# Performance work log

Measured on AMD Instinct MI355X. Metric: run time of the kernel, lower is better.

Reference implementation:

```python
import jax, jax.numpy as jnp
import numpy as np

NEG = -1e9
THRESH = 0.97


def _gat(x, emask, W, al, ar, b):
    # x: [B,N,Fin], emask: [B,N,N] bool (src,dst), W: [Fin,H*D], al/ar: [H,D], b: [H*D]
    B, N, _ = x.shape
    H, D = al.shape
    feat = (x @ W).reshape(B, N, H, D)
    el = jnp.einsum('bnhd,hd->bnh', feat, al)
    er = jnp.einsum('bnhd,hd->bnh', feat, ar)
    # DGL GATConv: e = leaky_relu(el[src] + er[dst]); edge softmax over incoming edges of dst
    e = jax.nn.leaky_relu(el[:, :, None, :] + er[:, None, :, :], 0.2)  # [B,src,dst,H]
    e = jnp.where(emask[..., None], e, NEG)
    a = jnp.where(emask[..., None], jax.nn.softmax(e, axis=1), 0.0)  # softmax over src
    rst = jnp.einsum('bsdh,bshf->bdhf', a, feat).reshape(B, N, H * D)
    return jax.nn.elu(rst + b)


def _sem_attention(z, nmask, W1, b1, W2):
    # z: [B,N,M,Dz]; masked mean over all valid nodes of the batched graph (== DGL batch semantics)
    p = jnp.tanh(z @ W1 + b1) @ W2  # [B,N,M,1]
    w = (p * nmask[:, :, None, None]).sum(axis=(0, 1)) / nmask.sum()  # [M,1]
    beta = jax.nn.softmax(w, axis=0)  # [M,1]
    return (beta[None, None] * z).sum(axis=2)  # [B,N,Dz]


def _han_layer(h, emasks, nmask, fc, al, ar, b, sW1, sb1, sW2):
    M = fc.shape[0]
    embs = [_gat(h, emasks[m], fc[m], al[m], ar[m], b[m]) for m in range(M)]
    z = jnp.stack(embs, axis=2)  # [B,N,M,H*D]
    return _sem_attention(z, nmask, sW1, sb1, sW2)


def setup_inputs() -> dict:
    key = jax.random.key(0)
    ks = jax.random.split(key, 24)
    B, M, N, Fin = 4, 5, 1000, 64
    H, D = 4, 64
    HD = H * D  # 256
    SH = 128    # semantic attention hidden
    OUT = 5
    s = 0.1
    inp = {
        'x': jax.random.normal(ks[0], (B, M, N, Fin), dtype=jnp.float32),
        'adj': jax.random.uniform(ks[1], (B, M, N, N), dtype=jnp.float32),
        'node_nums': jax.random.randint(ks[2], (B,), 0, N),
        # layer 1 (in = Fin)
        'gat_fc1': jax.random.normal(ks[3], (M, Fin, HD), dtype=jnp.float32) * s,
        'gat_al1': jax.random.normal(ks[4], (M, H, D), dtype=jnp.float32) * s,
        'gat_ar1': jax.random.normal(ks[5], (M, H, D), dtype=jnp.float32) * s,
        'gat_b1': jnp.zeros((M, HD), dtype=jnp.float32),
        'sem_W1_1': jax.random.normal(ks[6], (HD, SH), dtype=jnp.float32) * s,
        'sem_b1_1': jnp.zeros((SH,), dtype=jnp.float32),
        'sem_W2_1': jax.random.normal(ks[7], (SH, 1), dtype=jnp.float32) * s,
        # layer 2 (in = HD)
        'gat_fc2': jax.random.normal(ks[8], (M, HD, HD), dtype=jnp.float32) * s,
        'gat_al2': jax.random.normal(ks[9], (M, H, D), dtype=jnp.float32) * s,
        'gat_ar2': jax.random.normal(ks[10], (M, H, D), dtype=jnp.float32) * s,
        'gat_b2': jnp.zeros((M, HD), dtype=jnp.float32),
        'sem_W1_2': jax.random.normal(ks[11], (HD, SH), dtype=jnp.float32) * s,
        'sem_b1_2': jnp.zeros((SH,), dtype=jnp.float32),
        'sem_W2_2': jax.random.normal(ks[12], (SH, 1), dtype=jnp.float32) * s,
        # prediction head
        'pred_W': jax.random.normal(ks[13], (HD, OUT), dtype=jnp.float32) * s,
        'pred_b': jnp.zeros((OUT,), dtype=jnp.float32),
    }
    return inp


def reference(x, adj, node_nums, gat_fc1, gat_al1, gat_ar1, gat_b1,
              sem_W1_1, sem_b1_1, sem_W2_1,
              gat_fc2, gat_al2, gat_ar2, gat_b2,
              sem_W1_2, sem_b1_2, sem_W2_2,
              pred_W, pred_b):
    B, M, N, Fin = x.shape
    h = x[:, 0]  # original cat-then-[0]: only channel-0 features are used
    nmask = (jnp.arange(N)[None, :] < node_nums[:, None]).astype(x.dtype)  # [B,N]
    pair = (nmask[:, :, None] * nmask[:, None, :]) > 0  # [B,N,N]
    emasks = [(adj[:, m] > THRESH) & pair for m in range(M)]
    h = _han_layer(h, emasks, nmask, gat_fc1, gat_al1, gat_ar1, gat_b1,
                   sem_W1_1, sem_b1_1, sem_W2_1)
    h = _han_layer(h, emasks, nmask, gat_fc2, gat_al2, gat_ar2, gat_b2,
                   sem_W1_2, sem_b1_2, sem_W2_2)
    logits = (h @ pred_W + pred_b) * nmask[:, :, None]  # scatter into padded [B,N,OUT]
    return logits
```

## Files before the change

### kernel.cpp

```cpp
#include <hip/hip_runtime.h>
#include <hip/hip_bf16.h>

#define B_ 4
#define M_ 5
#define N_ 1000
#define FIN 64
#define H_ 4
#define D_ 64
#define HD 256
#define SH 128
#define OUTD 5
#define NW 16
#define THRESH_ 0.97f

typedef unsigned short u16;
typedef u16 us8 __attribute__((ext_vector_type(8)));
typedef short s16x8 __attribute__((ext_vector_type(8)));
typedef float f32x4 __attribute__((ext_vector_type(4)));

__device__ inline u16 bf16_bits(float v) {
  __hip_bfloat16 h = __float2bfloat16(v);
  return *reinterpret_cast<u16*>(&h);
}
__device__ inline float bf16_val(u16 b) {
  __hip_bfloat16 h;
  *reinterpret_cast<u16*>(&h) = b;
  return __bfloat162float(h);
}
__device__ inline float b2f(u16 u) {
  union { unsigned int i; float f; } c;
  c.i = ((unsigned int)u) << 16;
  return c.f;
}
__device__ inline void split2(float v, u16& h, u16& l) {
  h = bf16_bits(v);
  l = bf16_bits(v - bf16_val(h));
}
__device__ inline void beta_from_sums(const float* __restrict__ psum,
                                      const int* __restrict__ node_nums,
                                      float* bb) {
  float tot = (float)(node_nums[0] + node_nums[1] + node_nums[2] + node_nums[3]);
  float w[M_], mx = -1e30f;
#pragma unroll
  for (int m = 0; m < M_; ++m) {
    w[m] = psum[m] / tot;
    mx = fmaxf(mx, w[m]);
  }
  float s = 0.f;
#pragma unroll
  for (int m = 0; m < M_; ++m) {
    w[m] = __expf(w[m] - mx);
    s += w[m];
  }
  float inv = 1.f / s;
#pragma unroll
  for (int m = 0; m < M_; ++m) bb[m] = w[m] * inv;
}

__device__ void splitT_body(const float* __restrict__ s, u16* __restrict__ hiT,
                            u16* __restrict__ loT, int K, int N, int k0, int n0,
                            char* smem) {
  float(*tile)[33] = (float(*)[33])smem;
  int tid = threadIdx.x;
  int kl = tid >> 3, nq = (tid & 7) * 4;
  *(float4*)&tile[kl][nq] = *(const float4*)(s + (size_t)(k0 + kl) * N + n0 + nq);
  __syncthreads();
  int nl = tid >> 3, kq = (tid & 7) * 4;
  ushort4 h, l;
  split2(tile[kq + 0][nl], h.x, l.x);
  split2(tile[kq + 1][nl], h.y, l.y);
  split2(tile[kq + 2][nl], h.z, l.z);
  split2(tile[kq + 3][nl], h.w, l.w);
  size_t o = (size_t)(n0 + nl) * K + k0 + kq;
  *(ushort4*)(hiT + o) = h;
  *(ushort4*)(loT + o) = l;
}

__global__ __launch_bounds__(256) void prep_all(
    const float* __restrict__ adj, const int* __restrict__ node_nums,
    unsigned long long* __restrict__ maskW,
    const float* __restrict__ fc1, u16* __restrict__ fc1Th, u16* __restrict__ fc1Tl,
    const float* __restrict__ fc2, u16* __restrict__ fc2Th, u16* __restrict__ fc2Tl,
    const float* __restrict__ sW1_1, u16* __restrict__ sW1Th1, u16* __restrict__ sW1Tl1,
    const float* __restrict__ sW1_2, u16* __restrict__ sW1Th2, u16* __restrict__ sW1Tl2) {
  __shared__ __align__(16) char smem[4608];
  int bi = blockIdx.x;
  int tid = threadIdx.x;
  if (bi < 5120) {
    int bx = bi & 15, by = (bi >> 4) & 15, bm = bi >> 8;
    int b = bm / M_;
    int s0 = bx * 64, d0 = by * 64;
    int nn = node_nums[b];
    unsigned char(*tile)[65] = (unsigned char(*)[65])smem;
    const float* arow = adj + (size_t)bm * N_ * N_;
#pragma unroll
    for (int k = 0; k < 16; ++k) {
      int idx = k * 256 + tid;
      int sl = idx >> 6, dl = idx & 63;
      int s = s0 + sl, d = d0 + dl;
      unsigned char v = 0;
      if (s < nn && d < nn && s < N_ && d < N_)
        v = (arow[(size_t)s * N_ + d] > THRESH_) ? 1 : 0;
      tile[sl][dl] = v;
    }
    __syncthreads();
    int w = tid >> 6, lane = tid & 63;
#pragma unroll
    for (int j = 0; j < 16; ++j) {
      int dl = w * 16 + j;
      bool act = tile[lane][dl] != 0;
      unsigned long long word = __ballot(act);
      int d = d0 + dl;
      if (lane == 0 && d < N_)
        maskW[((size_t)bm * N_ + d) * NW + bx] = word;
    }
    return;
  }
  bi -= 5120;
  if (bi < 80) {
    int kx = bi % 2, ny = (bi / 2) % 8, z = bi / 16;
    splitT_body(fc1 + (size_t)z * FIN * HD, fc1Th + (size_t)z * HD * FIN,
                fc1Tl + (size_t)z * HD * FIN, FIN, HD, kx * 32, ny * 32, smem);
    return;
  }
  bi -= 80;
  if (bi < 320) {
    int kx = bi % 8, ny = (bi / 8) % 8, z = bi / 64;
    splitT_body(fc2 + (size_t)z * HD * HD, fc2Th + (size_t)z * HD * HD,
                fc2Tl + (size_t)z * HD * HD, HD, HD, kx * 32, ny * 32, smem);
    return;
  }
  bi -= 320;
  if (bi < 32) {
    int kx = bi % 8, ny = bi / 8;
    splitT_body(sW1_1, sW1Th1, sW1Tl1, HD, SH, kx * 32, ny * 32, smem);
    return;
  }
  bi -= 32;
  {
    int kx = bi % 8, ny = bi / 8;
    splitT_body(sW1_2, sW1Th2, sW1Tl2, HD, SH, kx * 32, ny * 32, smem);
  }
}

__global__ __launch_bounds__(256) void gemm_mfma3(
    const float* __restrict__ A, int Mz, size_t aZ,
    const u16* __restrict__ Bh, const u16* __restrict__ Bl, size_t bZ,
    float* __restrict__ C, u16* __restrict__ Cbf, size_t cZ,
    int Mrows, int K, int Nc,
    const float* __restrict__ al, const float* __restrict__ ar,
    float* __restrict__ el, float* __restrict__ er) {
  __shared__ u16 sAh[64][40], sAl[64][40], sBh[64][40], sBl[64][40];
  __shared__ float elbuf[64][2], erbuf[64][2];
  int z = blockIdx.z;
  int b = z / Mz, m = z % Mz;
  const float* Ab = A + (size_t)b * aZ;
  const u16* Bhb = Bh + (size_t)m * bZ;
  const u16* Blb = Bl + (size_t)m * bZ;
  float* Cb = C + (size_t)z * cZ;
  u16* Cfb = Cbf + (size_t)z * cZ;
  int row0 = blockIdx.x * 64, col0 = blockIdx.y * 64;
  int tid = threadIdx.x;
  int arow = tid >> 2, akq = (tid & 3) * 8;
  int wid = tid >> 6, lane = tid & 63;
  int wr = (wid >> 1) * 32, wc = (wid & 1) * 32;
  int lrow = lane & 15, kseg = (lane >> 4) * 8;
  f32x4 zero4 = {0.f, 0.f, 0.f, 0.f};
  f32x4 acc[2][2];
  acc[0][0] = zero4; acc[0][1] = zero4; acc[1][0] = zero4; acc[1][1] = zero4;
  for (int k0 = 0; k0 < K; k0 += 32) {
    float4 a0 = make_float4(0.f, 0.f, 0.f, 0.f), a1 = a0;
    int gr = row0 + arow;
    if (gr < Mrows) {
      const float* ap = Ab + (size_t)gr * K + k0 + akq;
      a0 = *(const float4*)ap;
      a1 = *(const float4*)(ap + 4);
    }
    us8 hv, lv;
    {
      u16 th, tl;
      split2(a0.x, th, tl); hv[0] = th; lv[0] = tl;
      split2(a0.y, th, tl); hv[1] = th; lv[1] = tl;
      split2(a0.z, th, tl); hv[2] = th; lv[2] = tl;
      split2(a0.w, th, tl); hv[3] = th; lv[3] = tl;
      split2(a1.x, th, tl); hv[4] = th; lv[4] = tl;
      split2(a1.y, th, tl); hv[5] = th; lv[5] = tl;
      split2(a1.z, th, tl); hv[6] = th; lv[6] = tl;
      split2(a1.w, th, tl); hv[7] = th; lv[7] = tl;
    }
    *(us8*)&sAh[arow][akq] = hv;
    *(us8*)&sAl[arow][akq] = lv;
    us8 bv = *(const us8*)(Bhb + (size_t)(col0 + arow) * K + k0 + akq);
    us8 blv = *(const us8*)(Blb + (size_t)(col0 + arow) * K + k0 + akq);
    *(us8*)&sBh[arow][akq] = bv;
    *(us8*)&sBl[arow][akq] = blv;
    __syncthreads();
    s16x8 aH[2], aL[2], bH[2], bL[2];
#pragma unroll
    for (int i = 0; i < 2; ++i) {
      aH[i] = *(const s16x8*)&sAh[wr + 16 * i + lrow][kseg];
      aL[i] = *(const s16x8*)&sAl[wr + 16 * i + lrow][kseg];
      bH[i] = *(const s16x8*)&sBh[wc + 16 * i + lrow][kseg];
      bL[i] = *(const s16x8*)&sBl[wc + 16 * i + lrow][kseg];
    }
#pragma unroll
    for (int i = 0; i < 2; ++i)
#pragma unroll
      for (int j = 0; j < 2; ++j) {
        acc[i][j] = __builtin_amdgcn_mfma_f32_16x16x32_bf16(aH[i], bH[j], acc[i][j], 0, 0, 0);
        acc[i][j] = __builtin_amdgcn_mfma_f32_16x16x32_bf16(aH[i], bL[j], acc[i][j], 0, 0, 0);
        acc[i][j] = __builtin_amdgcn_mfma_f32_16x16x32_bf16(aL[i], bH[j], acc[i][j], 0, 0, 0);
      }
    __syncthreads();
  }
#pragma unroll
  for (int i = 0; i < 2; ++i)
#pragma unroll
    for (int j = 0; j < 2; ++j) {
      int ccol = col0 + wc + 16 * j + lrow;
#pragma unroll
      for (int r = 0; r < 4; ++r) {
        int crow = row0 + wr + 16 * i + (lane >> 4) * 4 + r;
        if (crow < Mrows) {
          float v = acc[i][j][r];
          Cb[(size_t)crow * Nc + ccol] = v;
          Cfb[(size_t)crow * Nc + ccol] = bf16_bits(v);
        }
      }
    }
  float alv0 = al[m * HD + col0 + wc + lrow];
  float alv1 = al[m * HD + col0 + wc + 16 + lrow];
  float arv0 = ar[m * HD + col0 + wc + lrow];
  float arv1 = ar[m * HD + col0 + wc + 16 + lrow];
#pragma unroll
  for (int i = 0; i < 2; ++i)
#pragma unroll
    for (int r = 0; r < 4; ++r) {
      float pl = acc[i][0][r] * alv0 + acc[i][1][r] * alv1;
      float pr = acc[i][0][r] * arv0 + acc[i][1][r] * arv1;
#pragma unroll
      for (int s = 1; s < 16; s <<= 1) {
        pl += __shfl_xor(pl, s, 64);
        pr += __shfl_xor(pr, s, 64);
      }
      if (lrow == 0) {
        int rl = wr + 16 * i + (lane >> 4) * 4 + r;
        elbuf[rl][wc >> 5] = pl;
        erbuf[rl][wc >> 5] = pr;
      }
    }
  __syncthreads();
  if (tid < 64) {
    int grow = row0 + tid;
    if (grow < Mrows) {
      int h = col0 >> 6;
      size_t bmN = (size_t)(b * M_ + m) * N_;
      el[(bmN + grow) * H_ + h] = elbuf[tid][0] + elbuf[tid][1];
      er[(bmN + grow) * H_ + h] = erbuf[tid][0] + erbuf[tid][1];
    }
  }
}

__global__ __launch_bounds__(256) void gat_agg(
    const unsigned long long* __restrict__ maskW, const u16* __restrict__ featbf,
    const float* __restrict__ el, const float* __restrict__ er,
    const float* __restrict__ gb, float* __restrict__ zout,
    u16* __restrict__ zbh, float* __restrict__ psum) {
  int wid = threadIdx.x >> 6, lane = threadIdx.x & 63;
  const int NWGQ = (B_ * M_ * N_ / 4) / 8;
  int orig = blockIdx.x;
  if (orig == 0 && threadIdx.x < 8) psum[threadIdx.x] = 0.f;
  int bid = (orig & 7) * NWGQ + (orig >> 3);
  int gw = bid * 4 + wid;
  int d = gw % N_, bm = gw / N_;
  int m = bm % M_, b = bm / M_;
  __shared__ int slist_all[4][1024];
  int* slist = slist_all[wid];

  const unsigned long long* mrow = maskW + ((size_t)bm * N_ + d) * NW;
  int cnt = 0;
#pragma unroll
  for (int q = 0; q < NW / 2; ++q) {
    ulonglong2 wp = *(const ulonglong2*)(mrow + q * 2);
    unsigned long long w0 = wp.x, w1 = wp.y;
    if (w0) {
      if ((w0 >> lane) & 1ull) {
        int pos = cnt + (int)__popcll(w0 & ((1ull << lane) - 1ull));
        slist[pos] = q * 128 + lane;
      }
      cnt += (int)__popcll(w0);
    }
    if (w1) {
      if ((w1 >> lane) & 1ull) {
        int pos = cnt + (int)__popcll(w1 & ((1ull << lane) - 1ull));
        slist[pos] = q * 128 + 64 + lane;
      }
      cnt += (int)__popcll(w1);
    }
  }

  int h = lane >> 4;
  float4 bias4 = *(const float4*)(gb + m * HD + lane * 4);
  size_t zoff = ((size_t)(b * N_ + d) * M_ + m) * HD + lane * 4;
  float4 o;
  if (cnt == 0) {
    o.x = bias4.x > 0.f ? bias4.x : (__expf(bias4.x) - 1.f);
    o.y = bias4.y > 0.f ? bias4.y : (__expf(bias4.y) - 1.f);
    o.z = bias4.z > 0.f ? bias4.z : (__expf(bias4.z) - 1.f);
    o.w = bias4.w > 0.f ? bias4.w : (__expf(bias4.w) - 1.f);
  } else {
    if (lane < 4) slist[cnt + lane] = slist[0];
    size_t bmN = (size_t)bm * N_;
    float erv = er[(bmN + d) * H_ + h];
    const float* elb = el + bmN * H_;
    const u16* fbb = featbf + bmN * HD;
    int lane4 = lane * 4;
    float den0 = 0.f, den1 = 0.f, den2 = 0.f, den3 = 0.f;
    f32x4 A0 = {0.f, 0.f, 0.f, 0.f}, A1 = A0, A2 = A0, A3 = A0;
    for (int i = 0; i < cnt; i += 4) {
      int4 s4 = *(const int4*)&slist[i];
      float e0 = elb[(size_t)s4.x * H_ + h];
      float e1 = elb[(size_t)s4.y * H_ + h];
      float e2 = elb[(size_t)s4.z * H_ + h];
      float e3 = elb[(size_t)s4.w * H_ + h];
      ushort4 g0 = *(const ushort4*)(fbb + (size_t)s4.x * HD + lane4);
      ushort4 g1 = *(const ushort4*)(fbb + (size_t)s4.y * HD + lane4);
      ushort4 g2 = *(const ushort4*)(fbb + (size_t)s4.z * HD + lane4);
      ushort4 g3 = *(const ushort4*)(fbb + (size_t)s4.w * HD + lane4);
      float v0 = e0 + erv; v0 = v0 > 0.f ? v0 : 0.2f * v0;
      float v1 = e1 + erv; v1 = v1 > 0.f ? v1 : 0.2f * v1;
      float v2 = e2 + erv; v2 = v2 > 0.f ? v2 : 0.2f * v2;
      float v3 = e3 + erv; v3 = v3 > 0.f ? v3 : 0.2f * v3;
      float w0 = __expf(v0);
      float w1 = __expf(v1) * ((i + 1 < cnt) ? 1.f : 0.f);
      float w2 = __expf(v2) * ((i + 2 < cnt) ? 1.f : 0.f);
      float w3 = __expf(v3) * ((i + 3 < cnt) ? 1.f : 0.f);
      f32x4 f0 = {b2f(g0.x), b2f(g0.y), b2f(g0.z), b2f(g0.w)};
      f32x4 f1 = {b2f(g1.x), b2f(g1.y), b2f(g1.z), b2f(g1.w)};
      f32x4 f2 = {b2f(g2.x), b2f(g2.y), b2f(g2.z), b2f(g2.w)};
      f32x4 f3 = {b2f(g3.x), b2f(g3.y), b2f(g3.z), b2f(g3.w)};
      den0 += w0; den1 += w1; den2 += w2; den3 += w3;
      A0 += w0 * f0; A1 += w1 * f1; A2 += w2 * f2; A3 += w3 * f3;
    }
    float den = (den0 + den1) + (den2 + den3);
    f32x4 A = (A0 + A1) + (A2 + A3);
    float inv = 1.f / den;
    float vx = A[0] * inv + bias4.x;
    float vy = A[1] * inv + bias4.y;
    float vz = A[2] * inv + bias4.z;
    float vw = A[3] * inv + bias4.w;
    o.x = vx > 0.f ? vx : (__expf(vx) - 1.f);
    o.y = vy > 0.f ? vy : (__expf(vy) - 1.f);
    o.z = vz > 0.f ? vz : (__expf(vz) - 1.f);
    o.w = vw > 0.f ? vw : (__expf(vw) - 1.f);
  }
  *(float4*)(zout + zoff) = o;
  ushort4 hh;
  hh.x = bf16_bits(o.x);
  hh.y = bf16_bits(o.y);
  hh.z = bf16_bits(o.z);
  hh.w = bf16_bits(o.w);
  *(ushort4*)(zbh + zoff) = hh;
}

__global__ __launch_bounds__(256) void gemm_sem(
    const u16* __restrict__ Ah, const u16* __restrict__ Bh,
    const float* __restrict__ bias, const float* __restrict__ W2,
    float* __restrict__ psum, const int* __restrict__ node_nums, int Mrows) {
  __shared__ u16 sA[64][40], sB[64][40];
  __shared__ float redm[M_];
  int row0 = blockIdx.x * 64, col0 = blockIdx.y * 64;
  int tid = threadIdx.x;
  int arow = tid >> 2, akq = (tid & 3) * 8;
  int wid = tid >> 6, lane = tid & 63;
  int wr = (wid >> 1) * 32, wc = (wid & 1) * 32;
  int lrow = lane & 15, kseg = (lane >> 4) * 8;
  if (tid < M_) redm[tid] = 0.f;
  f32x4 zero4 = {0.f, 0.f, 0.f, 0.f};
  f32x4 acc[2][2];
  acc[0][0] = zero4; acc[0][1] = zero4; acc[1][0] = zero4; acc[1][1] = zero4;
  for (int k0 = 0; k0 < HD; k0 += 32) {
    us8 av = {0, 0, 0, 0, 0, 0, 0, 0};
    int gr = row0 + arow;
    if (gr < Mrows) av = *(const us8*)(Ah + (size_t)gr * HD + k0 + akq);
    *(us8*)&sA[arow][akq] = av;
    us8 bv = *(const us8*)(Bh + (size_t)(col0 + arow) * HD + k0 + akq);
    *(us8*)&sB[arow][akq] = bv;
    __syncthreads();
    s16x8 aH[2], bH[2];
#pragma unroll
    for (int i = 0; i < 2; ++i) {
      aH[i] = *(const s16x8*)&sA[wr + 16 * i + lrow][kseg];
      bH[i] = *(const s16x8*)&sB[wc + 16 * i + lrow][kseg];
    }
#pragma unroll
    for (int i = 0; i < 2; ++i)
#pragma unroll
      for (int j = 0; j < 2; ++j)
        acc[i][j] = __builtin_amdgcn_mfma_f32_16x16x32_bf16(aH[i], bH[j], acc[i][j], 0, 0, 0);
    __syncthreads();
  }
  int nn0 = node_nums[0], nn1 = node_nums[1], nn2 = node_nums[2], nn3 = node_nums[3];
#pragma unroll
  for (int i = 0; i < 2; ++i) {
#pragma unroll
    for (int r = 0; r < 4; ++r) {
      float part = 0.f;
#pragma unroll
      for (int j = 0; j < 2; ++j) {
        int ccol = col0 + wc + 16 * j + lrow;
        float v = tanhf(acc[i][j][r] + bias[ccol]);
        part += v * W2[ccol];
      }
#pragma unroll
      for (int s = 1; s < 16; s <<= 1) part += __shfl_xor(part, s, 64);
      int crow = row0 + wr + 16 * i + (lane >> 4) * 4 + r;
      if (lrow == 0 && crow < Mrows) {
        int m = crow % M_;
        int bn = crow / M_;
        int bb = bn / N_, n = bn % N_;
        int nn = (bb == 0) ? nn0 : (bb == 1) ? nn1 : (bb == 2) ? nn2 : nn3;
        if (n < nn) atomicAdd(&redm[m], part);
      }
    }
  }
  __syncthreads();
  if (tid < M_) atomicAdd(&psum[tid], redm[tid]);
}

__global__ __launch_bounds__(256) void sem_combine(const float* __restrict__ zb,
                                                   const float* __restrict__ psum,
                                                   const int* __restrict__ node_nums,
                                                   float* __restrict__ hout) {
  float bb[M_];
  beta_from_sums(psum, node_nums, bb);
  int idx = blockIdx.x * 256 + threadIdx.x;
  int hd = idx & (HD - 1);
  int bn = idx >> 8;
  const float* zr = zb + (size_t)bn * M_ * HD + hd;
  float v = bb[0] * zr[0] + bb[1] * zr[HD] + bb[2] * zr[2 * HD] +
            bb[3] * zr[3 * HD] + bb[4] * zr[4 * HD];
  hout[idx] = v;
}

__global__ __launch_bounds__(256) void sem_combine_pred(
    const float* __restrict__ zb, const float* __restrict__ psum,
    const int* __restrict__ node_nums, const float* __restrict__ W,
    const float* __restrict__ bias, float* __restrict__ out) {
  float bb[M_];
  beta_from_sums(psum, node_nums, bb);
  int row = blockIdx.x * 4 + (threadIdx.x >> 6);
  int lane = threadIdx.x & 63;
  int b = row / N_, n = row % N_;
  const float* zr = zb + (size_t)row * M_ * HD + lane * 4;
  float4 z0 = *(const float4*)(zr);
  float4 z1 = *(const float4*)(zr + HD);
  float4 z2 = *(const float4*)(zr + 2 * HD);
  float4 z3 = *(const float4*)(zr + 3 * HD);
  float4 z4 = *(const float4*)(zr + 4 * HD);
  float hx = bb[0] * z0.x + bb[1] * z1.x + bb[2] * z2.x + bb[3] * z3.x + bb[4] * z4.x;
  float hy = bb[0] * z0.y + bb[1] * z1.y + bb[2] * z2.y + bb[3] * z3.y + bb[4] * z4.y;
  float hz = bb[0] * z0.z + bb[1] * z1.z + bb[2] * z2.z + bb[3] * z3.z + bb[4] * z4.z;
  float hw = bb[0] * z0.w + bb[1] * z1.w + bb[2] * z2.w + bb[3] * z3.w + bb[4] * z4.w;
  int k = lane * 4;
  float res[OUTD];
#pragma unroll
  for (int o = 0; o < OUTD; ++o) {
    float v = hx * W[(k + 0) * OUTD + o] + hy * W[(k + 1) * OUTD + o] +
              hz * W[(k + 2) * OUTD + o] + hw * W[(k + 3) * OUTD + o];
#pragma unroll
    for (int s = 1; s < 64; s <<= 1) v += __shfl_xor(v, s, 64);
    res[o] = v;
  }
  if (lane == 0) {
    float nm = (n < node_nums[b]) ? 1.f : 0.f;
#pragma unroll
    for (int o = 0; o < OUTD; ++o)
      out[(size_t)row * OUTD + o] = (res[o] + bias[o]) * nm;
  }
}

extern "C" void kernel_launch(void* const* d_in, const int* in_sizes, int n_in,
                              void* d_out, int out_size, void* d_ws, size_t ws_size,
                              hipStream_t stream) {
  const float* x = (const float*)d_in[0];
  const float* adj = (const float*)d_in[1];
  const int* node_nums = (const int*)d_in[2];
  const float* fc1 = (const float*)d_in[3];
  const float* al1 = (const float*)d_in[4];
  const float* ar1 = (const float*)d_in[5];
  const float* gb1 = (const float*)d_in[6];
  const float* sW1_1 = (const float*)d_in[7];
  const float* sb1_1 = (const float*)d_in[8];
  const float* sW2_1 = (const float*)d_in[9];
  const float* fc2 = (const float*)d_in[10];
  const float* al2 = (const float*)d_in[11];
  const float* ar2 = (const float*)d_in[12];
  const float* gb2 = (const float*)d_in[13];
  const float* sW1_2 = (const float*)d_in[14];
  const float* sb1_2 = (const float*)d_in[15];
  const float* sW2_2 = (const float*)d_in[16];
  const float* predW = (const float*)d_in[17];
  const float* predb = (const float*)d_in[18];
  float* out = (float*)d_out;

  char* ws = (char*)d_ws;
  size_t off = 0;
  unsigned long long* maskW = (unsigned long long*)(ws + off);
  off += (size_t)B_ * M_ * N_ * NW * 8;
  float* feat = (float*)(ws + off); off += (size_t)B_ * M_ * N_ * HD * 4;
  u16* featbf = (u16*)(ws + off); off += (size_t)B_ * M_ * N_ * HD * 2;
  float* el = (float*)(ws + off); off += (size_t)B_ * M_ * N_ * H_ * 4;
  float* er = (float*)(ws + off); off += (size_t)B_ * M_ * N_ * H_ * 4;
  float* zb = (float*)(ws + off); off += (size_t)B_ * N_ * M_ * HD * 4;
  float* h1 = (float*)(ws + off); off += (size_t)B_ * N_ * HD * 4;
  float* psum = (float*)(ws + off); off += 64;
  u16* fc1Th = (u16*)(ws + off); off += (size_t)M_ * HD * FIN * 2;
  u16* fc1Tl = (u16*)(ws + off); off += (size_t)M_ * HD * FIN * 2;
  u16* fc2Th = (u16*)(ws + off); off += (size_t)M_ * HD * HD * 2;
  u16* fc2Tl = (u16*)(ws + off); off += (size_t)M_ * HD * HD * 2;
  u16* sW1Th1 = (u16*)(ws + off); off += (size_t)SH * HD * 2;
  u16* sW1Tl1 = (u16*)(ws + off); off += (size_t)SH * HD * 2;
  u16* sW1Th2 = (u16*)(ws + off); off += (size_t)SH * HD * 2;
  u16* sW1Tl2 = (u16*)(ws + off); off += (size_t)SH * HD * 2;
  u16* zbh = (u16*)(ws + off); off += (size_t)B_ * N_ * M_ * HD * 2;

  const int ROWS = B_ * N_ * M_;
  const int PREP_BLOCKS = 5120 + 80 + 320 + 32 + 32;

  prep_all<<<dim3(PREP_BLOCKS), 256, 0, stream>>>(
      adj, node_nums, maskW, fc1, fc1Th, fc1Tl, fc2, fc2Th, fc2Tl,
      sW1_1, sW1Th1, sW1Tl1, sW1_2, sW1Th2, sW1Tl2);

  gemm_mfma3<<<dim3(16, HD / 64, B_ * M_), 256, 0, stream>>>(
      x, M_, (size_t)M_ * N_ * FIN, fc1Th, fc1Tl, (size_t)HD * FIN,
      feat, featbf, (size_t)N_ * HD, N_, FIN, HD, al1, ar1, el, er);
  gat_agg<<<dim3(ROWS / 4), 256, 0, stream>>>(maskW, featbf, el, er, gb1, zb, zbh, psum);
  gemm_sem<<<dim3((ROWS + 63) / 64, SH / 64), 256, 0, stream>>>(
      zbh, sW1Th1, sb1_1, sW2_1, psum, node_nums, ROWS);
  sem_combine<<<dim3(B_ * N_ * HD / 256), 256, 0, stream>>>(zb, psum, node_nums, h1);

  gemm_mfma3<<<dim3(16, HD / 64, B_ * M_), 256, 0, stream>>>(
      h1, M_, (size_t)N_ * HD, fc2Th, fc2Tl, (size_t)HD * HD,
      feat, featbf, (size_t)N_ * HD, N_, HD, HD, al2, ar2, el, er);
  gat_agg<<<dim3(ROWS / 4), 256, 0, stream>>>(maskW, featbf, el, er, gb2, zb, zbh, psum);
  gemm_sem<<<dim3((ROWS + 63) / 64, SH / 64), 256, 0, stream>>>(
      zbh, sW1Th2, sb1_2, sW2_2, psum, node_nums, ROWS);
  sem_combine_pred<<<dim3(B_ * N_ / 4), 256, 0, stream>>>(
      zb, psum, node_nums, predW, predb, out);
}
```

Baseline: 172.1 us.

## Drop fp32 intermediate buffers and read bf16 copies in combine kernels

Removes the unused fp32 feature output from the projection GEMM and the fp32 per-metapath GAT output, so the semantic-combine and prediction kernels read the existing bf16 buffer instead. The source index list in shared memory shrinks from int to u16. This cuts global write and read traffic across several kernels. The cost is lower precision in the semantic combination, which now uses bf16-rounded inputs instead of fp32.

```diff
diff --git a/kernel.cpp b/kernel.cpp
--- a/kernel.cpp
+++ b/kernel.cpp
@@ -146,7 +146,7 @@
 __global__ __launch_bounds__(256) void gemm_mfma3(
     const float* __restrict__ A, int Mz, size_t aZ,
     const u16* __restrict__ Bh, const u16* __restrict__ Bl, size_t bZ,
-    float* __restrict__ C, u16* __restrict__ Cbf, size_t cZ,
+    u16* __restrict__ Cbf, size_t cZ,
     int Mrows, int K, int Nc,
     const float* __restrict__ al, const float* __restrict__ ar,
     float* __restrict__ el, float* __restrict__ er) {
@@ -157,7 +157,6 @@
   const float* Ab = A + (size_t)b * aZ;
   const u16* Bhb = Bh + (size_t)m * bZ;
   const u16* Blb = Bl + (size_t)m * bZ;
-  float* Cb = C + (size_t)z * cZ;
   u16* Cfb = Cbf + (size_t)z * cZ;
   int row0 = blockIdx.x * 64, col0 = blockIdx.y * 64;
   int tid = threadIdx.x;
@@ -221,11 +220,8 @@
 #pragma unroll
       for (int r = 0; r < 4; ++r) {
         int crow = row0 + wr + 16 * i + (lane >> 4) * 4 + r;
-        if (crow < Mrows) {
-          float v = acc[i][j][r];
-          Cb[(size_t)crow * Nc + ccol] = v;
-          Cfb[(size_t)crow * Nc + ccol] = bf16_bits(v);
-        }
+        if (crow < Mrows)
+          Cfb[(size_t)crow * Nc + ccol] = bf16_bits(acc[i][j][r]);
       }
     }
   float alv0 = al[m * HD + col0 + wc + lrow];
@@ -264,8 +260,8 @@
 __global__ __launch_bounds__(256) void gat_agg(
     const unsigned long long* __restrict__ maskW, const u16* __restrict__ featbf,
     const float* __restrict__ el, const float* __restrict__ er,
-    const float* __restrict__ gb, float* __restrict__ zout,
-    u16* __restrict__ zbh, float* __restrict__ psum) {
+    const float* __restrict__ gb, u16* __restrict__ zbh,
+    float* __restrict__ psum) {
   int wid = threadIdx.x >> 6, lane = threadIdx.x & 63;
   const int NWGQ = (B_ * M_ * N_ / 4) / 8;
   int orig = blockIdx.x;
@@ -274,8 +270,8 @@
   int gw = bid * 4 + wid;
   int d = gw % N_, bm = gw / N_;
   int m = bm % M_, b = bm / M_;
-  __shared__ int slist_all[4][1024];
-  int* slist = slist_all[wid];
+  __shared__ u16 slist_all[4][1032];
+  u16* slist = slist_all[wid];
 
   const unsigned long long* mrow = maskW + ((size_t)bm * N_ + d) * NW;
   int cnt = 0;
@@ -286,14 +282,14 @@
     if (w0) {
       if ((w0 >> lane) & 1ull) {
         int pos = cnt + (int)__popcll(w0 & ((1ull << lane) - 1ull));
-        slist[pos] = q * 128 + lane;
+        slist[pos] = (u16)(q * 128 + lane);
       }
       cnt += (int)__popcll(w0);
     }
     if (w1) {
       if ((w1 >> lane) & 1ull) {
         int pos = cnt + (int)__popcll(w1 & ((1ull << lane) - 1ull));
-        slist[pos] = q * 128 + 64 + lane;
+        slist[pos] = (u16)(q * 128 + 64 + lane);
       }
       cnt += (int)__popcll(w1);
     }
@@ -318,7 +314,7 @@
     float den0 = 0.f, den1 = 0.f, den2 = 0.f, den3 = 0.f;
     f32x4 A0 = {0.f, 0.f, 0.f, 0.f}, A1 = A0, A2 = A0, A3 = A0;
     for (int i = 0; i < cnt; i += 4) {
-      int4 s4 = *(const int4*)&slist[i];
+      ushort4 s4 = *(const ushort4*)&slist[i];
       float e0 = elb[(size_t)s4.x * H_ + h];
       float e1 = elb[(size_t)s4.y * H_ + h];
       float e2 = elb[(size_t)s4.z * H_ + h];
@@ -345,16 +341,15 @@
     float den = (den0 + den1) + (den2 + den3);
     f32x4 A = (A0 + A1) + (A2 + A3);
     float inv = 1.f / den;
-    float vx = A[0] * inv + bias4.x;
-    float vy = A[1] * inv + bias4.y;
-    float vz = A[2] * inv + bias4.z;
-    float vw = A[3] * inv + bias4.w;
-    o.x = vx > 0.f ? vx : (__expf(vx) - 1.f);
-    o.y = vy > 0.f ? vy : (__expf(vy) - 1.f);
-    o.z = vz > 0.f ? vz : (__expf(vz) - 1.f);
-    o.w = vw > 0.f ? vw : (__expf(vw) - 1.f);
-  }
-  *(float4*)(zout + zoff) = o;
+    o.x = A[0] * inv + bias4.x;
+    o.y = A[1] * inv + bias4.y;
+    o.z = A[2] * inv + bias4.z;
+    o.w = A[3] * inv + bias4.w;
+    o.x = o.x > 0.f ? o.x : (__expf(o.x) - 1.f);
+    o.y = o.y > 0.f ? o.y : (__expf(o.y) - 1.f);
+    o.z = o.z > 0.f ? o.z : (__expf(o.z) - 1.f);
+    o.w = o.w > 0.f ? o.w : (__expf(o.w) - 1.f);
+  }
   ushort4 hh;
   hh.x = bf16_bits(o.x);
   hh.y = bf16_bits(o.y);
@@ -428,23 +423,28 @@
   if (tid < M_) atomicAdd(&psum[tid], redm[tid]);
 }
 
-__global__ __launch_bounds__(256) void sem_combine(const float* __restrict__ zb,
+__global__ __launch_bounds__(256) void sem_combine(const u16* __restrict__ zbh,
                                                    const float* __restrict__ psum,
                                                    const int* __restrict__ node_nums,
                                                    float* __restrict__ hout) {
   float bb[M_];
   beta_from_sums(psum, node_nums, bb);
-  int idx = blockIdx.x * 256 + threadIdx.x;
-  int hd = idx & (HD - 1);
-  int bn = idx >> 8;
-  const float* zr = zb + (size_t)bn * M_ * HD + hd;
-  float v = bb[0] * zr[0] + bb[1] * zr[HD] + bb[2] * zr[2 * HD] +
-            bb[3] * zr[3 * HD] + bb[4] * zr[4 * HD];
-  hout[idx] = v;
+  int q = blockIdx.x * 256 + threadIdx.x;
+  int hd4 = (q & 63) * 4;
+  int bn = q >> 6;
+  const u16* zr = zbh + (size_t)bn * M_ * HD + hd4;
+  f32x4 acc = {0.f, 0.f, 0.f, 0.f};
+#pragma unroll
+  for (int m = 0; m < M_; ++m) {
+    ushort4 g = *(const ushort4*)(zr + m * HD);
+    f32x4 f = {b2f(g.x), b2f(g.y), b2f(g.z), b2f(g.w)};
+    acc += bb[m] * f;
+  }
+  *(f32x4*)(hout + (size_t)bn * HD + hd4) = acc;
 }
 
 __global__ __launch_bounds__(256) void sem_combine_pred(
-    const float* __restrict__ zb, const float* __restrict__ psum,
+    const u16* __restrict__ zbh, const float* __restrict__ psum,
     const int* __restrict__ node_nums, const float* __restrict__ W,
     const float* __restrict__ bias, float* __restrict__ out) {
   float bb[M_];
@@ -452,16 +452,16 @@
   int row = blockIdx.x * 4 + (threadIdx.x >> 6);
   int lane = threadIdx.x & 63;
   int b = row / N_, n = row % N_;
-  const float* zr = zb + (size_t)row * M_ * HD + lane * 4;
-  float4 z0 = *(const float4*)(zr);
-  float4 z1 = *(const float4*)(zr + HD);
-  float4 z2 = *(const float4*)(zr + 2 * HD);
-  float4 z3 = *(const float4*)(zr + 3 * HD);
-  float4 z4 = *(const float4*)(zr + 4 * HD);
-  float hx = bb[0] * z0.x + bb[1] * z1.x + bb[2] * z2.x + bb[3] * z3.x + bb[4] * z4.x;
-  float hy = bb[0] * z0.y + bb[1] * z1.y + bb[2] * z2.y + bb[3] * z3.y + bb[4] * z4.y;
-  float hz = bb[0] * z0.z + bb[1] * z1.z + bb[2] * z2.z + bb[3] * z3.z + bb[4] * z4.z;
-  float hw = bb[0] * z0.w + bb[1] * z1.w + bb[2] * z2.w + bb[3] * z3.w + bb[4] * z4.w;
+  const u16* zr = zbh + (size_t)row * M_ * HD + lane * 4;
+  float hx = 0.f, hy = 0.f, hz = 0.f, hw = 0.f;
+#pragma unroll
+  for (int m = 0; m < M_; ++m) {
+    ushort4 g = *(const ushort4*)(zr + m * HD);
+    hx += bb[m] * b2f(g.x);
+    hy += bb[m] * b2f(g.y);
+    hz += bb[m] * b2f(g.z);
+    hw += bb[m] * b2f(g.w);
+  }
   int k = lane * 4;
   float res[OUTD];
 #pragma unroll
@@ -508,11 +508,10 @@
   size_t off = 0;
   unsigned long long* maskW = (unsigned long long*)(ws + off);
   off += (size_t)B_ * M_ * N_ * NW * 8;
-  float* feat = (float*)(ws + off); off += (size_t)B_ * M_ * N_ * HD * 4;
   u16* featbf = (u16*)(ws + off); off += (size_t)B_ * M_ * N_ * HD * 2;
   float* el = (float*)(ws + off); off += (size_t)B_ * M_ * N_ * H_ * 4;
   float* er = (float*)(ws + off); off += (size_t)B_ * M_ * N_ * H_ * 4;
-  float* zb = (float*)(ws + off); off += (size_t)B_ * N_ * M_ * HD * 4;
+  u16* zbh = (u16*)(ws + off); off += (size_t)B_ * N_ * M_ * HD * 2;
   float* h1 = (float*)(ws + off); off += (size_t)B_ * N_ * HD * 4;
   float* psum = (float*)(ws + off); off += 64;
   u16* fc1Th = (u16*)(ws + off); off += (size_t)M_ * HD * FIN * 2;
@@ -523,7 +522,6 @@
   u16* sW1Tl1 = (u16*)(ws + off); off += (size_t)SH * HD * 2;
   u16* sW1Th2 = (u16*)(ws + off); off += (size_t)SH * HD * 2;
   u16* sW1Tl2 = (u16*)(ws + off); off += (size_t)SH * HD * 2;
-  u16* zbh = (u16*)(ws + off); off += (size_t)B_ * N_ * M_ * HD * 2;
 
   const int ROWS = B_ * N_ * M_;
   const int PREP_BLOCKS = 5120 + 80 + 320 + 32 + 32;
@@ -534,18 +532,18 @@
 
   gemm_mfma3<<<dim3(16, HD / 64, B_ * M_), 256, 0, stream>>>(
       x, M_, (size_t)M_ * N_ * FIN, fc1Th, fc1Tl, (size_t)HD * FIN,
-      feat, featbf, (size_t)N_ * HD, N_, FIN, HD, al1, ar1, el, er);
-  gat_agg<<<dim3(ROWS / 4), 256, 0, stream>>>(maskW, featbf, el, er, gb1, zb, zbh, psum);
+      featbf, (size_t)N_ * HD, N_, FIN, HD, al1, ar1, el, er);
+  gat_agg<<<dim3(ROWS / 4), 256, 0, stream>>>(maskW, featbf, el, er, gb1, zbh, psum);
   gemm_sem<<<dim3((ROWS + 63) / 64, SH / 64), 256, 0, stream>>>(
       zbh, sW1Th1, sb1_1, sW2_1, psum, node_nums, ROWS);
-  sem_combine<<<dim3(B_ * N_ * HD / 256), 256, 0, stream>>>(zb, psum, node_nums, h1);
+  sem_combine<<<dim3(B_ * N_ * HD / 1024), 256, 0, stream>>>(zbh, psum, node_nums, h1);
 
   gemm_mfma3<<<dim3(16, HD / 64, B_ * M_), 256, 0, stream>>>(
       h1, M_, (size_t)N_ * HD, fc2Th, fc2Tl, (size_t)HD * HD,
-      feat, featbf, (size_t)N_ * HD, N_, HD, HD, al2, ar2, el, er);
-  gat_agg<<<dim3(ROWS / 4), 256, 0, stream>>>(maskW, featbf, el, er, gb2, zb, zbh, psum);
+      featbf, (size_t)N_ * HD, N_, HD, HD, al2, ar2, el, er);
+  gat_agg<<<dim3(ROWS / 4), 256, 0, stream>>>(maskW, featbf, el, er, gb2, zbh, psum);
   gemm_sem<<<dim3((ROWS + 63) / 64, SH / 64), 256, 0, stream>>>(
       zbh, sW1Th2, sb1_2, sW2_2, psum, node_nums, ROWS);
   sem_combine_pred<<<dim3(B_ * N_ / 4), 256, 0, stream>>>(
-      zb, psum, node_nums, predW, predb, out);
-}
+      zbh, psum, node_nums, predW, predb, out);
+}
```

Result: faster. 164.6 us, median of 2 (-4.3%).
